# Kernel tuning notes

Hardware: AMD Instinct MI355X
Metric: run time of the kernel (lower is better)

Reference implementation:

```python
import jax, jax.numpy as jnp
import numpy as np

B, C, H, W = 4, 64, 256, 256
DS = 4        # ClusterLocalAtt downscale
CS = 2        # FastClusterAtt cluster_stride
NH = 4        # FastClusterAtt num_heads
G = 4         # OrthoConvClustering groups
N_NOISE = 8   # number of -1 (noise) labels; even and divisible by B


def _maxpool(x, k):
    b, c, h, w = x.shape
    return x.reshape(b, c, h // k, k, w // k, k).max(axis=(3, 5))


def _normalize(x, eps=1e-12):
    n = jnp.linalg.norm(x, axis=-1, keepdims=True)
    return x / jnp.maximum(n, eps)


def _feat_sim(cf, nf):
    # cf: (B,k,HW), nf: (B,n,HW) -> (B,k) mean cosine similarity over noise rows
    return jnp.einsum('bkl,bnl->bkn', _normalize(cf), _normalize(nf)).mean(-1)


def setup_inputs():
    key = jax.random.key(0)
    ks = jax.random.split(key, 12)
    x = jax.random.normal(ks[0], (B, C, H, W), jnp.float32)
    noise_idx = jnp.arange(N_NOISE, dtype=jnp.int32)
    labels = jax.random.randint(ks[1], (B * C,), 0, 12, dtype=jnp.int32)
    labels = labels.at[noise_idx].set(-1)
    inv = 1.0 / np.sqrt(C // G)
    return {
        'x': x, 'labels': labels, 'noise_idx': noise_idx,
        'qkv_w1': jax.random.normal(ks[2], (3 * C,), jnp.float32) * 0.5,
        'qkv_b1': jax.random.normal(ks[3], (3 * C,), jnp.float32) * 0.1,
        'up_k': jax.random.normal(ks[4], (C, DS, DS), jnp.float32) * 0.25,
        'up_b': jax.random.normal(ks[5], (C,), jnp.float32) * 0.1,
        'clu_w': jax.random.normal(ks[6], (G, C // G, C // G), jnp.float32) * inv,
        'clu_b': jnp.zeros((C,), jnp.float32),
        'qkv_w2': jax.random.normal(ks[7], (3 * C,), jnp.float32) * 0.5,
        'bais_w': jax.random.normal(ks[8], (C, C), jnp.float32) * (inv * 0.5),
        'bais_b': jax.random.normal(ks[9], (C,), jnp.float32) * 0.1,
    }


def reference(x, labels, noise_idx, qkv_w1, qkv_b1, up_k, up_b,
              clu_w, clu_b, qkv_w2, bais_w, bais_b):
    idx3 = jnp.arange(3 * C) // 3  # grouped 1x1 conv (groups=C): out ch j reads in ch j//3
    # ================= ClusterLocalAtt =================
    x_down = _maxpool(x, DS)                        # (B,C,Hd,Wd)
    Hd, Wd = H // DS, W // DS
    hw = Hd * Wd
    qkv = x_down[:, idx3] * qkv_w1[None, :, None, None] + qkv_b1[None, :, None, None]
    qkv = qkv.reshape(3 * B * C, hw)                # torch: reshape(1, 3*B*C, hw)
    q, k, v = jnp.split(qkv, 3, axis=0)             # each (B*C, hw) - batch/ch mixed, faithful
    valid = labels != -1
    allowed = (labels[:, None] == labels[None, :]) & valid[:, None] & valid[None, :]
    scores = q @ k.T                                # (BC, BC)
    attn = jax.nn.softmax(jnp.where(allowed, scores, -1e30), axis=-1)
    att = jnp.where(valid[:, None], attn @ v, 0.0)  # noise rows stay zero
    out = att.reshape(B, C, Hd, Wd)
    # depthwise ConvTranspose2d(kernel=DS, stride=DS): each input px -> DSxDS block
    up = jnp.einsum('bchw,cpq->bchpwq', out, up_k).reshape(B, C, H, W)
    up = up + up_b[None, :, None, None]
    noise = x.reshape(B * C, H * W)[noise_idx].reshape(B, N_NOISE // B, H * W)
    sim = _feat_sim(up.reshape(B, C, H * W), noise)[:, :, None, None]  # (B,C,1,1)
    out_clu = x + (up + (1.0 - sim) * x)
    # ================= FastClusterAtt =================
    xf = out_clu.reshape(B, G, C // G, H * W)
    xc = jnp.einsum('goi,bgil->bgol', clu_w, xf).reshape(B, C, H * W) + clu_b[None, :, None]
    x_ds = _maxpool(xc.reshape(B, C, H, W), CS)     # (B,C,Hs,Ws)
    Hs, Ws = H // CS, W // CS
    Ls = Hs * Ws
    qkv2 = (x_ds[:, idx3] * qkv_w2[None, :, None, None]).reshape(B, 3, NH, C // NH, Ls)
    qh, kh, vh = qkv2[:, 0], qkv2[:, 1], qkv2[:, 2]  # (B,NH,hd,Ls)
    sc = (qh * kh).sum(axis=2, keepdims=True) / np.sqrt(C // NH)  # (B,NH,1,Ls)
    a = jax.nn.softmax(sc, axis=-1)
    oh = (a * vh).sum(axis=-1).reshape(B, C)        # (B,C) global pooled heads
    # bilinear upsample of a spatially-constant map is the same constant -> skip interp
    ov = jnp.einsum('oc,bc->bo', bais_w, oh) + bais_b
    out_full = jnp.broadcast_to(ov[:, :, None, None], (B, C, H, W))
    sim2 = _feat_sim(out_full.reshape(B, C, H * W), noise)[:, :, None, None]
    WWT = jnp.einsum('goi,gpi->gop', clu_w, clu_w)
    I = jnp.eye(C // G, dtype=clu_w.dtype)
    ortho = 1.0 - jax.lax.stop_gradient(jnp.mean((WWT - I) ** 2))
    out2 = out_full * (1.0 - sim2) + ortho * out_clu
    return out_clu + out2
```

## Files before the change

### kernel.cpp

```cpp
#include <hip/hip_runtime.h>
#include <math.h>

#define WS_XD     0u
#define WS_S      1048576u
#define WS_GPART  1048832u
#define WS_G      2097408u
#define WS_COEF   2113792u
#define WS_CONST  2138368u
#define WS_ATT    2138624u
#define WS_FAC    3187200u
#define WS_XDS    3187456u
#define WS_ALPHA  7382016u
#define WS_BETA   7382272u
#define WS_NSTAT  7382273u
#define WS_P2     7382304u

__device__ __forceinline__ float bsum(float v, float* sd, int tid) {
    sd[tid] = v; __syncthreads();
    for (int off = 128; off > 0; off >>= 1) {
        if (tid < off) sd[tid] += sd[tid + off];
        __syncthreads();
    }
    float r = sd[0]; __syncthreads(); return r;
}
__device__ __forceinline__ float bmax(float v, float* sd, int tid) {
    sd[tid] = v; __syncthreads();
    for (int off = 128; off > 0; off >>= 1) {
        if (tid < off) sd[tid] = fmaxf(sd[tid], sd[tid + off]);
        __syncthreads();
    }
    float r = sd[0]; __syncthreads(); return r;
}

__global__ __launch_bounds__(256) void k_pool4(const float* __restrict__ x,
                                               const int* __restrict__ nidx,
                                               float* __restrict__ ws) {
    __shared__ float sd[256];
    int r = blockIdx.x, tid = threadIdx.x;
    const float4* xr = (const float4*)x + (size_t)r * 16384;
    float* xd = ws + WS_XD + (size_t)r * 4096;
    float sum = 0.f, s = 0.f, ss = 0.f;
    for (int it = 0; it < 16; ++it) {
        int o = it * 256 + tid;
        int h = o >> 6, w = o & 63;
        float m = -INFINITY;
        #pragma unroll
        for (int p = 0; p < 4; ++p) {
            float4 v = xr[(4 * h + p) * 64 + w];
            m = fmaxf(m, fmaxf(fmaxf(v.x, v.y), fmaxf(v.z, v.w)));
            s  += v.x + v.y + v.z + v.w;
            ss += v.x*v.x + v.y*v.y + v.z*v.z + v.w*v.w;
        }
        xd[o] = m; sum += m;
    }
    float st = bsum(sum, sd, tid);
    if (tid == 0) ws[WS_S + r] = st;
    bool isn = false;
    #pragma unroll
    for (int n = 0; n < 8; ++n) isn = isn || (nidx[n] == r);
    if (isn) {
        float ts = bsum(s, sd, tid);
        float tss = bsum(ss, sd, tid);
        if (tid == 0) {
            for (int n = 0; n < 8; ++n)
                if (nidx[n] == r) { ws[WS_NSTAT + n] = ts; ws[WS_NSTAT + 8 + n] = sqrtf(tss); }
        }
    }
}

__global__ __launch_bounds__(256) void k_gram(float* __restrict__ ws) {
    __shared__ __align__(16) float As[64][68];
    __shared__ __align__(16) float Bs[64][68];
    int tid = threadIdx.x, tx = tid & 15, ty = tid >> 4;
    int ra0 = blockIdx.y * 64, rb0 = 80 + blockIdx.x * 64, k0 = blockIdx.z * 64;
    const float4* xd4 = (const float4*)(ws + WS_XD);
    #pragma unroll
    for (int q = 0; q < 4; ++q) {
        int idx = q * 256 + tid;
        int row = idx >> 4, cf = idx & 15;
        float4 a = xd4[(size_t)(ra0 + row) * 1024 + (k0 >> 2) + cf];
        As[cf*4+0][row] = a.x; As[cf*4+1][row] = a.y; As[cf*4+2][row] = a.z; As[cf*4+3][row] = a.w;
        float4 b = xd4[(size_t)(rb0 + row) * 1024 + (k0 >> 2) + cf];
        Bs[cf*4+0][row] = b.x; Bs[cf*4+1][row] = b.y; Bs[cf*4+2][row] = b.z; Bs[cf*4+3][row] = b.w;
    }
    __syncthreads();
    float acc[4][4] = {};
    #pragma unroll 4
    for (int kk = 0; kk < 64; ++kk) {
        float4 a = *(const float4*)&As[kk][ty * 4];
        float4 b = *(const float4*)&Bs[kk][tx * 4];
        acc[0][0] += a.x*b.x; acc[0][1] += a.x*b.y; acc[0][2] += a.x*b.z; acc[0][3] += a.x*b.w;
        acc[1][0] += a.y*b.x; acc[1][1] += a.y*b.y; acc[1][2] += a.y*b.z; acc[1][3] += a.y*b.w;
        acc[2][0] += a.z*b.x; acc[2][1] += a.z*b.y; acc[2][2] += a.z*b.z; acc[2][3] += a.z*b.w;
        acc[3][0] += a.w*b.x; acc[3][1] += a.w*b.y; acc[3][2] += a.w*b.z; acc[3][3] += a.w*b.w;
    }
    float* gp = ws + WS_GPART + (size_t)blockIdx.z * 16384;
    #pragma unroll
    for (int i = 0; i < 4; ++i) {
        float4 o = make_float4(acc[i][0], acc[i][1], acc[i][2], acc[i][3]);
        *(float4*)&gp[(size_t)(ra0 + ty * 4 + i) * 128 + blockIdx.x * 64 + tx * 4] = o;
    }
}

__global__ __launch_bounds__(256) void k_gred(float* __restrict__ ws) {
    int t = blockIdx.x * 256 + threadIdx.x;
    const float4* gp = (const float4*)(ws + WS_GPART);
    float4 s = make_float4(0.f, 0.f, 0.f, 0.f);
    for (int p = 0; p < 64; ++p) {
        float4 v = gp[(size_t)p * 4096 + t];
        s.x += v.x; s.y += v.y; s.z += v.z; s.w += v.w;
    }
    ((float4*)(ws + WS_G))[t] = s;
}

__global__ __launch_bounds__(256) void k_attn1(const int* __restrict__ labels,
                                               const float* __restrict__ w1,
                                               const float* __restrict__ b1,
                                               float* __restrict__ ws) {
    __shared__ float sd[256];
    __shared__ float attn_s[256];
    int i = blockIdx.x, tid = threadIdx.x;
    int labi = labels[i];
    bool validi = (labi != -1);
    int bi = (i >= 192) ? 1 : 0;
    int ji = i - bi * 192;
    int rq = bi * 64 + ji / 3;
    float wq = w1[ji], bq = b1[ji];
    int gk = 256 + tid;
    int bk = (gk >= 384) ? 2 : 1;
    int jk = gk - bk * 192;
    int rk = bk * 64 + jk / 3;
    float wk = w1[jk], bbk = b1[jk];
    int labj = labels[tid];
    bool allowed = validi && (labj == labi) && (labj != -1);
    float score = wq * wk * ws[WS_G + rq * 128 + (rk - 80)]
                + wq * bbk * ws[WS_S + rq]
                + wk * bq  * ws[WS_S + rk]
                + 4096.0f * bq * bbk;
    float sc = allowed ? score : -1e30f;
    float m = bmax(sc, sd, tid);
    float e = __expf(sc - m);
    float Z = bsum(e, sd, tid);
    float attn = validi ? (e / Z) : 0.0f;
    attn_s[tid] = attn;
    int gv = 512 + tid;
    int bv = (gv >= 576) ? 3 : 2;
    int jv = gv - bv * 192;
    float csum = bsum(attn * b1[jv], sd, tid);
    if (tid < 96) {
        float s = 0.0f;
        if (tid < 86) {
            int rv = 170 + tid;
            int lo, hi, jadd;
            if (rv < 192) { int c = rv - 128; lo = 3 * c; if (lo < 128) lo = 128; hi = 3 * c + 2; jadd = -128; }
            else          { int c = rv - 192; lo = 3 * c; hi = 3 * c + 2; jadd = 64; }
            for (int jj = lo; jj <= hi; ++jj) s += attn_s[jj + jadd] * w1[jj];
        }
        ws[WS_COEF + i * 96 + tid] = s;
    }
    if (tid == 0) ws[WS_CONST + i] = csum;
}

__global__ __launch_bounds__(256) void k_attmm(float* __restrict__ ws) {
    __shared__ __align__(16) float As[96][68];
    __shared__ __align__(16) float Bs[96][64];
    int tid = threadIdx.x, tx = tid & 15, ty = tid >> 4;
    int col0 = blockIdx.x * 64, row0 = blockIdx.y * 64;
    const float4* cf4 = (const float4*)(ws + WS_COEF);
    const float4* xd4 = (const float4*)(ws + WS_XD);
    #pragma unroll
    for (int q = 0; q < 6; ++q) {
        int f = q * 256 + tid;
        {
            int row = f / 24, c24 = f - row * 24;
            float4 v = cf4[(size_t)(row0 + row) * 24 + c24];
            As[c24*4+0][row] = v.x; As[c24*4+1][row] = v.y; As[c24*4+2][row] = v.z; As[c24*4+3][row] = v.w;
        }
        {
            int row = f >> 4, c16 = f & 15;
            float4 v = make_float4(0.f, 0.f, 0.f, 0.f);
            if (row < 86) v = xd4[(size_t)(170 + row) * 1024 + (col0 >> 2) + c16];
            *(float4*)&Bs[row][c16 * 4] = v;
        }
    }
    __syncthreads();
    float acc[4][4] = {};
    #pragma unroll 4
    for (int kk = 0; kk < 96; ++kk) {
        float4 a = *(const float4*)&As[kk][ty * 4];
        float4 b = *(const float4*)&Bs[kk][tx * 4];
        acc[0][0] += a.x*b.x; acc[0][1] += a.x*b.y; acc[0][2] += a.x*b.z; acc[0][3] += a.x*b.w;
        acc[1][0] += a.y*b.x; acc[1][1] += a.y*b.y; acc[1][2] += a.y*b.z; acc[1][3] += a.y*b.w;
        acc[2][0] += a.z*b.x; acc[2][1] += a.z*b.y; acc[2][2] += a.z*b.z; acc[2][3] += a.z*b.w;
        acc[3][0] += a.w*b.x; acc[3][1] += a.w*b.y; acc[3][2] += a.w*b.z; acc[3][3] += a.w*b.w;
    }
    float* att = ws + WS_ATT;
    #pragma unroll
    for (int i = 0; i < 4; ++i) {
        int row = row0 + ty * 4 + i;
        float cv = ws[WS_CONST + row];
        float4 o = make_float4(acc[i][0] + cv, acc[i][1] + cv, acc[i][2] + cv, acc[i][3] + cv);
        *(float4*)&att[(size_t)row * 4096 + col0 + tx * 4] = o;
    }
}

__global__ __launch_bounds__(256) void k_sim(const float* __restrict__ x,
                                             const int* __restrict__ nidx,
                                             const float* __restrict__ upk,
                                             const float* __restrict__ upb,
                                             float* __restrict__ ws) {
    __shared__ float sd[256];
    int r = blockIdx.x, tid = threadIdx.x;
    int b = r >> 6, c = r & 63;
    const float* att = ws + WS_ATT + (size_t)r * 4096;
    const float4* xn0 = (const float4*)x + (size_t)nidx[2 * b] * 16384;
    const float4* xn1 = (const float4*)x + (size_t)nidx[2 * b + 1] * 16384;
    const float4* k4p = (const float4*)upk + c * 4;
    float ub = upb[c];
    float4 kk0 = k4p[0], kk1 = k4p[1], kk2 = k4p[2], kk3 = k4p[3];
    float s2 = 0.f, d0 = 0.f, d1 = 0.f;
    for (int it = 0; it < 64; ++it) {
        int f = it * 256 + tid;
        int rowf = f >> 6, c4 = f & 63;
        float av = att[(rowf >> 2) * 64 + c4];
        int p = rowf & 3;
        float4 kv = (p == 0) ? kk0 : ((p == 1) ? kk1 : ((p == 2) ? kk2 : kk3));
        float4 a0 = xn0[f], a1 = xn1[f];
        float u;
        u = av * kv.x + ub; s2 += u * u; d0 += u * a0.x; d1 += u * a1.x;
        u = av * kv.y + ub; s2 += u * u; d0 += u * a0.y; d1 += u * a1.y;
        u = av * kv.z + ub; s2 += u * u; d0 += u * a0.z; d1 += u * a1.z;
        u = av * kv.w + ub; s2 += u * u; d0 += u * a0.w; d1 += u * a1.w;
    }
    s2 = bsum(s2, sd, tid);
    d0 = bsum(d0, sd, tid);
    d1 = bsum(d1, sd, tid);
    if (tid == 0) {
        float nup = fmaxf(sqrtf(s2), 1e-12f);
        float n0 = fmaxf(ws[WS_NSTAT + 8 + 2 * b], 1e-12f);
        float n1 = fmaxf(ws[WS_NSTAT + 8 + 2 * b + 1], 1e-12f);
        float sim = 0.5f * (d0 / (nup * n0) + d1 / (nup * n1));
        ws[WS_FAC + r] = 2.0f - sim;
    }
}

__global__ __launch_bounds__(256) void k_cluds(const float* __restrict__ x,
                                               const float* __restrict__ upk,
                                               const float* __restrict__ upb,
                                               const float* __restrict__ cw,
                                               const float* __restrict__ cb,
                                               float* __restrict__ ws) {
    __shared__ float wcl[256];
    __shared__ float kup[256];
    __shared__ float cbl[16], ubl[16], fcl[16];
    int h2 = blockIdx.x, g = blockIdx.y, b = blockIdx.z;
    int t = threadIdx.x;
    wcl[t] = cw[g * 256 + t];
    kup[t] = upk[g * 256 + t];
    if (t < 16) {
        cbl[t] = cb[g * 16 + t];
        ubl[t] = upb[g * 16 + t];
        fcl[t] = ws[WS_FAC + b * 64 + g * 16 + t];
    }
    __syncthreads();
    int r0 = 2 * h2;
    int h_att = h2 >> 1, p0 = r0 & 3;
    int wa = t >> 2, q = t & 3;
    float oc0[16], oc1[16];
    const float* attb = ws + WS_ATT;
    #pragma unroll
    for (int i = 0; i < 16; ++i) {
        int cch = g * 16 + i;
        float av = attb[(size_t)(b * 64 + cch) * 4096 + h_att * 64 + wa];
        float u0 = av * kup[i * 16 + p0 * 4 + q] + ubl[i];
        float u1 = av * kup[i * 16 + (p0 + 1) * 4 + q] + ubl[i];
        const float* xrow = x + (size_t)(b * 64 + cch) * 65536;
        float x0 = xrow[r0 * 256 + t];
        float x1 = xrow[(r0 + 1) * 256 + t];
        oc0[i] = u0 + fcl[i] * x0;
        oc1[i] = u1 + fcl[i] * x1;
    }
    float* xds = ws + WS_XDS;
    #pragma unroll
    for (int o = 0; o < 16; ++o) {
        float a0 = cbl[o], a1 = cbl[o];
        #pragma unroll
        for (int i = 0; i < 16; ++i) {
            a0 += wcl[o * 16 + i] * oc0[i];
            a1 += wcl[o * 16 + i] * oc1[i];
        }
        float m = fmaxf(a0, a1);
        m = fmaxf(m, __shfl_xor(m, 1));
        if ((t & 1) == 0)
            xds[(size_t)((b * 64 + g * 16 + o) * 128 + h2) * 128 + (t >> 1)] = m;
    }
}

__global__ __launch_bounds__(256) void k_attn2a(const float* __restrict__ w2,
                                                float* __restrict__ ws) {
    __shared__ float ms[256], dsh[256];
    __shared__ float ns[256][16];
    int chunk = blockIdx.x, nh = blockIdx.y, b = blockIdx.z, tid = threadIdx.x;
    const float* X = ws + WS_XDS + (size_t)b * 1048576;
    float wqd[16], wkd[16], wvd[16];
    int oq[16], ok[16], ovo[16];
    #pragma unroll
    for (int d = 0; d < 16; ++d) {
        int jq = nh * 16 + d, jk = 64 + nh * 16 + d, jv = 128 + nh * 16 + d;
        wqd[d] = w2[jq]; wkd[d] = w2[jk]; wvd[d] = w2[jv];
        oq[d] = (jq / 3) * 16384; ok[d] = (jk / 3) * 16384; ovo[d] = (jv / 3) * 16384;
    }
    float m = -INFINITY, den = 0.f, num[16];
    #pragma unroll
    for (int d = 0; d < 16; ++d) num[d] = 0.f;
    #pragma unroll
    for (int e = 0; e < 2; ++e) {
        int l = chunk * 512 + e * 256 + tid;
        float sc = 0.f;
        #pragma unroll
        for (int d = 0; d < 16; ++d) sc += (X[oq[d] + l] * wqd[d]) * (X[ok[d] + l] * wkd[d]);
        sc *= 0.25f;
        float nm = fmaxf(m, sc);
        float rr = __expf(m - nm), ee = __expf(sc - nm);
        den = den * rr + ee;
        #pragma unroll
        for (int d = 0; d < 16; ++d) num[d] = num[d] * rr + ee * (X[ovo[d] + l] * wvd[d]);
        m = nm;
    }
    ms[tid] = m; dsh[tid] = den;
    #pragma unroll
    for (int d = 0; d < 16; ++d) ns[tid][d] = num[d];
    __syncthreads();
    for (int off = 128; off > 0; off >>= 1) {
        if (tid < off) {
            float ma = ms[tid], mb = ms[tid + off];
            float M = fmaxf(ma, mb);
            float ra = __expf(ma - M), rb = __expf(mb - M);
            dsh[tid] = dsh[tid] * ra + dsh[tid + off] * rb;
            #pragma unroll
            for (int d = 0; d < 16; ++d)
                ns[tid][d] = ns[tid][d] * ra + ns[tid + off][d] * rb;
            ms[tid] = M;
        }
        __syncthreads();
    }
    if (tid == 0) {
        float* p = ws + WS_P2 + ((size_t)(b * 4 + nh) * 32 + chunk) * 18;
        p[0] = ms[0]; p[1] = dsh[0];
        #pragma unroll
        for (int d = 0; d < 16; ++d) p[2 + d] = ns[0][d];
    }
}

__global__ __launch_bounds__(256) void k_tail(const float* __restrict__ bw,
                                              const float* __restrict__ bb,
                                              const float* __restrict__ cw,
                                              float* __restrict__ ws) {
    __shared__ float ohs[256], sd[256];
    int tid = threadIdx.x;
    int grp = tid >> 4;
    int j = tid & 15;
    float m = -INFINITY, den = 0.f, num[16];
    #pragma unroll
    for (int d = 0; d < 16; ++d) num[d] = 0.f;
    #pragma unroll
    for (int u = 0; u < 2; ++u) {
        const float* p = ws + WS_P2 + ((size_t)grp * 32 + j * 2 + u) * 18;
        float mo = p[0], dn = p[1];
        float M = fmaxf(m, mo);
        float ra = __expf(m - M), rb = __expf(mo - M);
        den = den * ra + dn * rb;
        #pragma unroll
        for (int d = 0; d < 16; ++d) num[d] = num[d] * ra + p[2 + d] * rb;
        m = M;
    }
    #pragma unroll
    for (int mask = 1; mask <= 8; mask <<= 1) {
        float mo = __shfl_xor(m, mask);
        float dn = __shfl_xor(den, mask);
        float M = fmaxf(m, mo);
        float ra = __expf(m - M), rb = __expf(mo - M);
        den = den * ra + dn * rb;
        #pragma unroll
        for (int d = 0; d < 16; ++d)
            num[d] = num[d] * ra + __shfl_xor(num[d], mask) * rb;
        m = M;
    }
    if (j == 0) {
        int b = grp >> 2, nh = grp & 3;
        #pragma unroll
        for (int d = 0; d < 16; ++d) ohs[b * 64 + nh * 16 + d] = num[d] / den;
    }
    __syncthreads();
    int b = tid >> 6, o = tid & 63;
    float s = bb[o];
    #pragma unroll 4
    for (int c2 = 0; c2 < 64; ++c2) s += bw[o * 64 + c2] * ohs[b * 64 + c2];
    float oacc = 0.f;
    for (int u = 0; u < 4; ++u) {
        int e = tid * 4 + u;
        int g = e >> 8, oo = (e >> 4) & 15, p = e & 15;
        float ss = 0.f;
        #pragma unroll
        for (int i = 0; i < 16; ++i) ss += cw[g * 256 + oo * 16 + i] * cw[g * 256 + p * 16 + i];
        float dd = ss - ((oo == p) ? 1.0f : 0.0f);
        oacc += dd * dd;
    }
    float tot = bsum(oacc, sd, tid);
    float nd = fmaxf(fabsf(s) * 256.0f, 1e-12f);
    float t0 = ws[WS_NSTAT + 2 * b], t1 = ws[WS_NSTAT + 2 * b + 1];
    float n0 = fmaxf(ws[WS_NSTAT + 8 + 2 * b], 1e-12f);
    float n1 = fmaxf(ws[WS_NSTAT + 8 + 2 * b + 1], 1e-12f);
    float sim2 = (s / nd) * 0.5f * (t0 / n0 + t1 / n1);
    ws[WS_ALPHA + tid] = (1.0f - sim2) * s;
    if (tid == 0) ws[WS_BETA] = 2.0f - tot / 1024.0f;
}

__global__ __launch_bounds__(256) void k_final(const float* __restrict__ x,
                                               const float* __restrict__ upk,
                                               const float* __restrict__ upb,
                                               const float* __restrict__ ws,
                                               float* __restrict__ out) {
    int idx = blockIdx.x * 256 + threadIdx.x;
    int r = idx >> 14;
    int rem = idx & 16383;
    int rowf = rem >> 6, c4 = rem & 63;
    int c = r & 63;
    float av = ws[WS_ATT + (size_t)r * 4096 + (rowf >> 2) * 64 + c4];
    int p = rowf & 3;
    float4 kv = ((const float4*)upk)[c * 4 + p];
    float ub = upb[c];
    float fac = ws[WS_FAC + r], al = ws[WS_ALPHA + r], be = ws[WS_BETA];
    float4 xv = ((const float4*)x)[idx];
    float4 o;
    o.x = be * (av * kv.x + ub + fac * xv.x) + al;
    o.y = be * (av * kv.y + ub + fac * xv.y) + al;
    o.z = be * (av * kv.z + ub + fac * xv.z) + al;
    o.w = be * (av * kv.w + ub + fac * xv.w) + al;
    ((float4*)out)[idx] = o;
}

extern "C" void kernel_launch(void* const* d_in, const int* in_sizes, int n_in,
                              void* d_out, int out_size, void* d_ws, size_t ws_size,
                              hipStream_t stream) {
    const float* x      = (const float*)d_in[0];
    const int*   labels = (const int*)d_in[1];
    const int*   nidx   = (const int*)d_in[2];
    const float* w1     = (const float*)d_in[3];
    const float* b1     = (const float*)d_in[4];
    const float* upk    = (const float*)d_in[5];
    const float* upb    = (const float*)d_in[6];
    const float* cw     = (const float*)d_in[7];
    const float* cb     = (const float*)d_in[8];
    const float* w2     = (const float*)d_in[9];
    const float* bw     = (const float*)d_in[10];
    const float* bb     = (const float*)d_in[11];
    float* ws  = (float*)d_ws;
    float* out = (float*)d_out;

    hipLaunchKernelGGL(k_pool4,  dim3(256),        dim3(256), 0, stream, x, nidx, ws);
    hipLaunchKernelGGL(k_gram,   dim3(2, 2, 64),   dim3(256), 0, stream, ws);
    hipLaunchKernelGGL(k_gred,   dim3(16),         dim3(256), 0, stream, ws);
    hipLaunchKernelGGL(k_attn1,  dim3(256),        dim3(256), 0, stream, labels, w1, b1, ws);
    hipLaunchKernelGGL(k_attmm,  dim3(64, 4),      dim3(256), 0, stream, ws);
    hipLaunchKernelGGL(k_sim,    dim3(256),        dim3(256), 0, stream, x, nidx, upk, upb, ws);
    hipLaunchKernelGGL(k_cluds,  dim3(128, 4, 4),  dim3(256), 0, stream, x, upk, upb, cw, cb, ws);
    hipLaunchKernelGGL(k_attn2a, dim3(32, 4, 4),   dim3(256), 0, stream, w2, ws);
    hipLaunchKernelGGL(k_tail,   dim3(1),          dim3(256), 0, stream, bw, bb, cw, ws);
    hipLaunchKernelGGL(k_final,  dim3(16384),      dim3(256), 0, stream, x, upk, upb, ws, out);
}
```

Measured before the change: 112.2 us.

## Fuse gram reduction into attn1, widen cluds per-thread work, vectorize attn2a

Removes the k_gred kernel by having k_attn1 reduce the 64 partial gram slices for its own row into shared memory. k_cluds now uses 128 threads, each handling a 2x2 output patch with float2 loads, which drops the shuffle and the half-idle stores. k_attn2a reads float4 vectors so each thread covers 4 positions, halving the chunk grid and the partial buffer, and k_tail no longer merges pairs. The cost is redundant partial-gram reads across attn1 blocks (rows repeat per query row), and fewer threads overall in cluds and attn2a.

```diff
diff --git a/kernel.cpp b/kernel.cpp
--- a/kernel.cpp
+++ b/kernel.cpp
@@ -4,7 +4,6 @@
 #define WS_XD     0u
 #define WS_S      1048576u
 #define WS_GPART  1048832u
-#define WS_G      2097408u
 #define WS_COEF   2113792u
 #define WS_CONST  2138368u
 #define WS_ATT    2138624u
@@ -102,29 +101,27 @@
     }
 }
 
-__global__ __launch_bounds__(256) void k_gred(float* __restrict__ ws) {
-    int t = blockIdx.x * 256 + threadIdx.x;
-    const float4* gp = (const float4*)(ws + WS_GPART);
-    float4 s = make_float4(0.f, 0.f, 0.f, 0.f);
-    for (int p = 0; p < 64; ++p) {
-        float4 v = gp[(size_t)p * 4096 + t];
-        s.x += v.x; s.y += v.y; s.z += v.z; s.w += v.w;
-    }
-    ((float4*)(ws + WS_G))[t] = s;
-}
-
 __global__ __launch_bounds__(256) void k_attn1(const int* __restrict__ labels,
                                                const float* __restrict__ w1,
                                                const float* __restrict__ b1,
                                                float* __restrict__ ws) {
     __shared__ float sd[256];
     __shared__ float attn_s[256];
+    __shared__ float grow[128];
     int i = blockIdx.x, tid = threadIdx.x;
     int labi = labels[i];
     bool validi = (labi != -1);
     int bi = (i >= 192) ? 1 : 0;
     int ji = i - bi * 192;
     int rq = bi * 64 + ji / 3;
+    if (tid < 128) {
+        const float* gp = ws + WS_GPART + (size_t)rq * 128 + tid;
+        float acc = 0.f;
+        #pragma unroll 8
+        for (int p = 0; p < 64; ++p) acc += gp[(size_t)p * 16384];
+        grow[tid] = acc;
+    }
+    __syncthreads();
     float wq = w1[ji], bq = b1[ji];
     int gk = 256 + tid;
     int bk = (gk >= 384) ? 2 : 1;
@@ -133,7 +130,7 @@
     float wk = w1[jk], bbk = b1[jk];
     int labj = labels[tid];
     bool allowed = validi && (labj == labi) && (labj != -1);
-    float score = wq * wk * ws[WS_G + rq * 128 + (rk - 80)]
+    float score = wq * wk * grow[rk - 80]
                 + wq * bbk * ws[WS_S + rq]
                 + wk * bq  * ws[WS_S + rk]
                 + 4096.0f * bq * bbk;
@@ -244,7 +241,7 @@
     }
 }
 
-__global__ __launch_bounds__(256) void k_cluds(const float* __restrict__ x,
+__global__ __launch_bounds__(128) void k_cluds(const float* __restrict__ x,
                                                const float* __restrict__ upk,
                                                const float* __restrict__ upb,
                                                const float* __restrict__ cw,
@@ -255,8 +252,8 @@
     __shared__ float cbl[16], ubl[16], fcl[16];
     int h2 = blockIdx.x, g = blockIdx.y, b = blockIdx.z;
     int t = threadIdx.x;
-    wcl[t] = cw[g * 256 + t];
-    kup[t] = upk[g * 256 + t];
+    wcl[t] = cw[g * 256 + t];       wcl[t + 128] = cw[g * 256 + t + 128];
+    kup[t] = upk[g * 256 + t];      kup[t + 128] = upk[g * 256 + t + 128];
     if (t < 16) {
         cbl[t] = cb[g * 16 + t];
         ubl[t] = upb[g * 16 + t];
@@ -264,68 +261,70 @@
     }
     __syncthreads();
     int r0 = 2 * h2;
-    int h_att = h2 >> 1, p0 = r0 & 3;
-    int wa = t >> 2, q = t & 3;
-    float oc0[16], oc1[16];
+    int p0 = r0 & 3;
+    int q0 = (2 * t) & 3;
+    int h_att = h2 >> 1;
+    int wa = t >> 1;
     const float* attb = ws + WS_ATT;
+    float oc[16][4];
     #pragma unroll
     for (int i = 0; i < 16; ++i) {
-        int cch = g * 16 + i;
-        float av = attb[(size_t)(b * 64 + cch) * 4096 + h_att * 64 + wa];
-        float u0 = av * kup[i * 16 + p0 * 4 + q] + ubl[i];
-        float u1 = av * kup[i * 16 + (p0 + 1) * 4 + q] + ubl[i];
-        const float* xrow = x + (size_t)(b * 64 + cch) * 65536;
-        float x0 = xrow[r0 * 256 + t];
-        float x1 = xrow[(r0 + 1) * 256 + t];
-        oc0[i] = u0 + fcl[i] * x0;
-        oc1[i] = u1 + fcl[i] * x1;
+        int ch = g * 16 + i;
+        float av = attb[(size_t)(b * 64 + ch) * 4096 + h_att * 64 + wa];
+        const float* xc = x + (size_t)(b * 64 + ch) * 65536;
+        float2 x0 = *(const float2*)&xc[r0 * 256 + 2 * t];
+        float2 x1 = *(const float2*)&xc[(r0 + 1) * 256 + 2 * t];
+        float ub = ubl[i], fc = fcl[i];
+        oc[i][0] = av * kup[i * 16 + p0 * 4 + q0]           + ub + fc * x0.x;
+        oc[i][1] = av * kup[i * 16 + p0 * 4 + q0 + 1]       + ub + fc * x0.y;
+        oc[i][2] = av * kup[i * 16 + (p0 + 1) * 4 + q0]     + ub + fc * x1.x;
+        oc[i][3] = av * kup[i * 16 + (p0 + 1) * 4 + q0 + 1] + ub + fc * x1.y;
     }
     float* xds = ws + WS_XDS;
     #pragma unroll
     for (int o = 0; o < 16; ++o) {
-        float a0 = cbl[o], a1 = cbl[o];
+        float cbv = cbl[o];
+        float a0 = cbv, a1 = cbv, a2 = cbv, a3 = cbv;
         #pragma unroll
         for (int i = 0; i < 16; ++i) {
-            a0 += wcl[o * 16 + i] * oc0[i];
-            a1 += wcl[o * 16 + i] * oc1[i];
-        }
-        float m = fmaxf(a0, a1);
-        m = fmaxf(m, __shfl_xor(m, 1));
-        if ((t & 1) == 0)
-            xds[(size_t)((b * 64 + g * 16 + o) * 128 + h2) * 128 + (t >> 1)] = m;
+            float wv = wcl[o * 16 + i];
+            a0 += wv * oc[i][0]; a1 += wv * oc[i][1];
+            a2 += wv * oc[i][2]; a3 += wv * oc[i][3];
+        }
+        float m = fmaxf(fmaxf(a0, a1), fmaxf(a2, a3));
+        xds[(size_t)((b * 64 + g * 16 + o) * 128 + h2) * 128 + t] = m;
     }
 }
 
 __global__ __launch_bounds__(256) void k_attn2a(const float* __restrict__ w2,
                                                 float* __restrict__ ws) {
+    __shared__ float wl2[192];
     __shared__ float ms[256], dsh[256];
-    __shared__ float ns[256][16];
+    __shared__ float ns[256][17];
     int chunk = blockIdx.x, nh = blockIdx.y, b = blockIdx.z, tid = threadIdx.x;
-    const float* X = ws + WS_XDS + (size_t)b * 1048576;
-    float wqd[16], wkd[16], wvd[16];
-    int oq[16], ok[16], ovo[16];
+    if (tid < 192) wl2[tid] = w2[tid];
+    __syncthreads();
+    const float4* X4 = (const float4*)(ws + WS_XDS + (size_t)b * 1048576);
+    int li = chunk * 256 + tid;
+    float4 sc = make_float4(0.f, 0.f, 0.f, 0.f);
     #pragma unroll
     for (int d = 0; d < 16; ++d) {
-        int jq = nh * 16 + d, jk = 64 + nh * 16 + d, jv = 128 + nh * 16 + d;
-        wqd[d] = w2[jq]; wkd[d] = w2[jk]; wvd[d] = w2[jv];
-        oq[d] = (jq / 3) * 16384; ok[d] = (jk / 3) * 16384; ovo[d] = (jv / 3) * 16384;
-    }
-    float m = -INFINITY, den = 0.f, num[16];
-    #pragma unroll
-    for (int d = 0; d < 16; ++d) num[d] = 0.f;
-    #pragma unroll
-    for (int e = 0; e < 2; ++e) {
-        int l = chunk * 512 + e * 256 + tid;
-        float sc = 0.f;
-        #pragma unroll
-        for (int d = 0; d < 16; ++d) sc += (X[oq[d] + l] * wqd[d]) * (X[ok[d] + l] * wkd[d]);
-        sc *= 0.25f;
-        float nm = fmaxf(m, sc);
-        float rr = __expf(m - nm), ee = __expf(sc - nm);
-        den = den * rr + ee;
-        #pragma unroll
-        for (int d = 0; d < 16; ++d) num[d] = num[d] * rr + ee * (X[ovo[d] + l] * wvd[d]);
-        m = nm;
+        int jq = nh * 16 + d, jk = 64 + nh * 16 + d;
+        float4 q4 = X4[(size_t)(jq / 3) * 4096 + li];
+        float4 k4 = X4[(size_t)(jk / 3) * 4096 + li];
+        float wqk = wl2[jq] * wl2[jk] * 0.25f;
+        sc.x += wqk * q4.x * k4.x; sc.y += wqk * q4.y * k4.y;
+        sc.z += wqk * q4.z * k4.z; sc.w += wqk * q4.w * k4.w;
+    }
+    float m = fmaxf(fmaxf(sc.x, sc.y), fmaxf(sc.z, sc.w));
+    float p0 = __expf(sc.x - m), p1 = __expf(sc.y - m), p2 = __expf(sc.z - m), p3 = __expf(sc.w - m);
+    float den = p0 + p1 + p2 + p3;
+    float num[16];
+    #pragma unroll
+    for (int d = 0; d < 16; ++d) {
+        int jv = 128 + nh * 16 + d;
+        float4 v4 = X4[(size_t)(jv / 3) * 4096 + li];
+        num[d] = wl2[jv] * (p0 * v4.x + p1 * v4.y + p2 * v4.z + p3 * v4.w);
     }
     ms[tid] = m; dsh[tid] = den;
     #pragma unroll
@@ -345,7 +344,7 @@
         __syncthreads();
     }
     if (tid == 0) {
-        float* p = ws + WS_P2 + ((size_t)(b * 4 + nh) * 32 + chunk) * 18;
+        float* p = ws + WS_P2 + ((size_t)(b * 4 + nh) * 16 + chunk) * 18;
         p[0] = ms[0]; p[1] = dsh[0];
         #pragma unroll
         for (int d = 0; d < 16; ++d) p[2 + d] = ns[0][d];
@@ -360,20 +359,10 @@
     int tid = threadIdx.x;
     int grp = tid >> 4;
     int j = tid & 15;
-    float m = -INFINITY, den = 0.f, num[16];
-    #pragma unroll
-    for (int d = 0; d < 16; ++d) num[d] = 0.f;
-    #pragma unroll
-    for (int u = 0; u < 2; ++u) {
-        const float* p = ws + WS_P2 + ((size_t)grp * 32 + j * 2 + u) * 18;
-        float mo = p[0], dn = p[1];
-        float M = fmaxf(m, mo);
-        float ra = __expf(m - M), rb = __expf(mo - M);
-        den = den * ra + dn * rb;
-        #pragma unroll
-        for (int d = 0; d < 16; ++d) num[d] = num[d] * ra + p[2 + d] * rb;
-        m = M;
-    }
+    const float* p = ws + WS_P2 + ((size_t)grp * 16 + j) * 18;
+    float m = p[0], den = p[1], num[16];
+    #pragma unroll
+    for (int d = 0; d < 16; ++d) num[d] = p[2 + d];
     #pragma unroll
     for (int mask = 1; mask <= 8; mask <<= 1) {
         float mo = __shfl_xor(m, mask);
@@ -399,11 +388,11 @@
     float oacc = 0.f;
     for (int u = 0; u < 4; ++u) {
         int e = tid * 4 + u;
-        int g = e >> 8, oo = (e >> 4) & 15, p = e & 15;
-        float ss = 0.f;
-        #pragma unroll
-        for (int i = 0; i < 16; ++i) ss += cw[g * 256 + oo * 16 + i] * cw[g * 256 + p * 16 + i];
-        float dd = ss - ((oo == p) ? 1.0f : 0.0f);
+        int g = e >> 8, oo = (e >> 4) & 15, pp = e & 15;
+        float ssv = 0.f;
+        #pragma unroll
+        for (int i = 0; i < 16; ++i) ssv += cw[g * 256 + oo * 16 + i] * cw[g * 256 + pp * 16 + i];
+        float dd = ssv - ((oo == pp) ? 1.0f : 0.0f);
         oacc += dd * dd;
     }
     float tot = bsum(oacc, sd, tid);
@@ -460,12 +449,11 @@
 
     hipLaunchKernelGGL(k_pool4,  dim3(256),        dim3(256), 0, stream, x, nidx, ws);
     hipLaunchKernelGGL(k_gram,   dim3(2, 2, 64),   dim3(256), 0, stream, ws);
-    hipLaunchKernelGGL(k_gred,   dim3(16),         dim3(256), 0, stream, ws);
     hipLaunchKernelGGL(k_attn1,  dim3(256),        dim3(256), 0, stream, labels, w1, b1, ws);
     hipLaunchKernelGGL(k_attmm,  dim3(64, 4),      dim3(256), 0, stream, ws);
     hipLaunchKernelGGL(k_sim,    dim3(256),        dim3(256), 0, stream, x, nidx, upk, upb, ws);
-    hipLaunchKernelGGL(k_cluds,  dim3(128, 4, 4),  dim3(256), 0, stream, x, upk, upb, cw, cb, ws);
-    hipLaunchKernelGGL(k_attn2a, dim3(32, 4, 4),   dim3(256), 0, stream, w2, ws);
+    hipLaunchKernelGGL(k_cluds,  dim3(128, 4, 4),  dim3(128), 0, stream, x, upk, upb, cw, cb, ws);
+    hipLaunchKernelGGL(k_attn2a, dim3(16, 4, 4),   dim3(256), 0, stream, w2, ws);
     hipLaunchKernelGGL(k_tail,   dim3(1),          dim3(256), 0, stream, bw, bb, cw, ws);
     hipLaunchKernelGGL(k_final,  dim3(16384),      dim3(256), 0, stream, x, upk, upb, ws, out);
 }
```

New measurement: 107.9 us. 3.8% less time.
